# Kernel tuning notes

Hardware: AMD Instinct MI355X
Metric: run time of the kernel (lower is better)

## Reference

```python
import jax, jax.numpy as jnp
import numpy as np

ALPHA = 0.99
EPS = 1e-12
INIT_HI = -60.0
INIT_LO = -90.0
VAR0 = 40.0 ** 2


def setup_inputs() -> dict:
    key = jax.random.key(0)
    x = jax.random.normal(key, (256, 4000, 64), dtype=jnp.float32)
    return {"x": x}


def reference(x) -> jnp.ndarray:
    B, T, F = x.shape
    step = (INIT_LO - INIT_HI) / (F - 1)
    mu0 = INIT_HI + jnp.arange(F, dtype=x.dtype) * step          # [F]
    mu0 = jnp.broadcast_to(mu0[None, :], (B, F))                  # [B, F]
    var0 = jnp.full((B, F), VAR0, dtype=x.dtype)

    def scan_step(carry, xt):
        mu, var = carry
        mu = ALPHA * mu + (1.0 - ALPHA) * xt
        var = ALPHA * var + (1.0 - ALPHA) * (xt - mu) ** 2        # dynamic_var=True
        out = (xt - mu) / (jnp.sqrt(var) + EPS)
        return (mu, var), out

    xt_seq = jnp.swapaxes(x, 0, 1)                                # [T, B, F]
    _, out_seq = jax.lax.scan(scan_step, (mu0, var0), xt_seq)
    return jnp.swapaxes(out_seq, 0, 1)                            # [B, T, F]
```

## Files before the change

kernel.cpp:

```cpp
#include <hip/hip_runtime.h>
#include <math.h>

#define ALPHA   0.99f
#define ONE_M   0.01f
#define T_LEN   4000
#define F_DIM   64
#define TT      160
#define NTILE   25
#define LTC     5
#define NC      32
#define NPC     5
#define NTHREADS 512
#define ROWF    68

typedef float f32x4 __attribute__((ext_vector_type(4)));

#define LGKM_BAR()                                                    \
  do { asm volatile("s_waitcnt lgkmcnt(0)" ::: "memory");             \
       __builtin_amdgcn_sched_barrier(0);                             \
       __builtin_amdgcn_s_barrier();                                  \
       __builtin_amdgcn_sched_barrier(0); } while (0)

#define TILE_BODY(VC, VN, kk)                                               \
  {                                                                         \
    const size_t tb = bbase + (size_t)(kk) * TT * F_DIM;                    \
                    \
    _Pragma("unroll")                                                       \
    for (int r = 0; r < NPC; ++r) {                                         \
      const int t = r * NC + c;                                             \
      *(f32x4*)&s_img[t * ROWF + g * 4] = VC[r];                            \
    }                                                                       \
    LGKM_BAR();                                                             \
    \
    f32x4 vX[LTC];                                                          \
    _Pragma("unroll")                                                       \
    for (int j = 0; j < LTC; ++j)                                           \
      vX[j] = *(const f32x4*)&s_img[(LTC * c + j) * ROWF + g * 4];          \
    if ((kk) + 1 < NTILE) {                                                 \
      _Pragma("unroll")                                                     \
      for (int r = 0; r < NPC; ++r)                                         \
        VN[r] = *(const f32x4*)(x + tb + (size_t)TT * F_DIM                 \
                                + (size_t)tid * 4 + (size_t)r * 2048);      \
    }                                                                       \
    f32x4 m = 0.f, sp = 0.f, su = 0.f;                                      \
    _Pragma("unroll")                                                       \
    for (int j = 0; j < LTC; ++j) {                                         \
      f32x4 xi = vX[j];                                                     \
      m = ALPHA * m + ONE_M * xi;                                           \
      f32x4 u = xi - m;                                                     \
      sp = ALPHA * sp + ONE_M * (u * u);                                    \
      su = su + u;                                                          \
    }                                                                       \
    *(f32x4*)&s_m [c * F_DIM + g * 4] = m;                                  \
    *(f32x4*)&s_sp[c * F_DIM + g * 4] = sp;                                 \
    *(f32x4*)&s_su[c * F_DIM + g * 4] = su;                                 \
    LGKM_BAR();                                                             \
       \
    if (tid < F_DIM) {                                                      \
      float mu = cmu, var = cvar;                                           \
      for (int cc = 0; cc < NC; ++cc) {                                     \
        float mm = s_m [cc * F_DIM + tid];                                  \
        float pp = s_sp[cc * F_DIM + tid];                                  \
        float uu = s_su[cc * F_DIM + tid];                                  \
        s_m [cc * F_DIM + tid] = mu;                    \
        s_sp[cc * F_DIM + tid] = var;                                       \
        float mun = AL * mu + mm;                                           \
        var = AL * var + pp + (C2 * uu) * mu + RR * mu * mu;                \
        mu = mun;                                                           \
      }                                                                     \
      cmu = mu; cvar = var;                                                 \
    }                                                                       \
    LGKM_BAR();                                                             \
     \
    f32x4 mu2  = *(const f32x4*)&s_m [c * F_DIM + g * 4];                   \
    f32x4 var2 = *(const f32x4*)&s_sp[c * F_DIM + g * 4];                   \
    _Pragma("unroll")                                                       \
    for (int j = 0; j < LTC; ++j) {                                         \
      f32x4 xi = vX[j];                                                     \
      mu2 = ALPHA * mu2 + ONE_M * xi;                                       \
      f32x4 d = xi - mu2;                                                   \
      var2 = ALPHA * var2 + ONE_M * (d * d);                                \
      f32x4 o;                                                              \
      o[0] = d[0] * __builtin_amdgcn_rsqf(var2[0]);                         \
      o[1] = d[1] * __builtin_amdgcn_rsqf(var2[1]);                         \
      o[2] = d[2] * __builtin_amdgcn_rsqf(var2[2]);                         \
      o[3] = d[3] * __builtin_amdgcn_rsqf(var2[3]);                         \
      *(f32x4*)&s_img[(LTC * c + j) * ROWF + g * 4] = o;                    \
    }                                                                       \
    LGKM_BAR();                                                             \
            \
    _Pragma("unroll")                                                       \
    for (int r = 0; r < NPC; ++r) {                                         \
      const int t = r * NC + c;                                             \
      f32x4 oc = *(const f32x4*)&s_img[t * ROWF + g * 4];                   \
      *(f32x4*)(out + tb + (size_t)tid * 4 + (size_t)r * 2048) = oc;        \
    }                                                                       \
    LGKM_BAR();           \
  }

__global__ __launch_bounds__(NTHREADS, 2)
void erbnorm_kernel(const float* __restrict__ x, float* __restrict__ out, float aL) {
    const int b   = blockIdx.x;
    const int tid = threadIdx.x;
    const int c   = tid >> 4;
    const int g   = tid & 15;

    const float AL = aL;
    const float C2 = -2.f * ONE_M * aL;
    const float RR = ALPHA * aL * (1.f - aL);

    __shared__ __align__(16) float s_img[TT * ROWF];
    __shared__ float s_m [NC * F_DIM];
    __shared__ float s_sp[NC * F_DIM];
    __shared__ float s_su[NC * F_DIM];

    const size_t bbase = (size_t)b * T_LEN * F_DIM;

    float cmu  = -60.f + (float)tid * (-30.f / 63.f);
    float cvar = 1600.f;

    f32x4 vA[NPC], vB[NPC];
#pragma unroll
    for (int r = 0; r < NPC; ++r)
        vA[r] = *(const f32x4*)(x + bbase + (size_t)tid * 4 + (size_t)r * 2048);

    for (int k2 = 0; k2 < NTILE - 1; k2 += 2) {
        TILE_BODY(vA, vB, k2);
        TILE_BODY(vB, vA, k2 + 1);
    }
    TILE_BODY(vA, vB, NTILE - 1);
}

extern "C" void kernel_launch(void* const* d_in, const int* in_sizes, int n_in,
                              void* d_out, int out_size, void* d_ws, size_t ws_size,
                              hipStream_t stream) {
    const float* x = (const float*)d_in[0];
    float* out = (float*)d_out;
    const float aL = (float)pow(0.99, (double)LTC);
    hipLaunchKernelGGL(erbnorm_kernel, dim3(256), dim3(NTHREADS), 0, stream,
                       x, out, aL);
}
```

Baseline: 110.4 us.

## Give each wave a private LDS slab to replace block barriers with wave fences

The global load/store mapping is rearranged so each wave handles a contiguous 20-timestep slab that matches the 4 chunks it scans. The transpose through LDS can then use a per-wave slab with only a wave-local lgkmcnt wait, which removes two block-wide barriers per tile. The next-tile prefetch is issued at the top of the tile, and launch bounds now ask for 4 blocks per CU. The raised occupancy target may force register spilling, and only the two barriers around the serial cross-chunk scan remain.

```diff
diff --git a/kernel.cpp b/kernel.cpp
--- a/kernel.cpp
+++ b/kernel.cpp
@@ -12,6 +12,7 @@
 #define NPC     5
 #define NTHREADS 512
 #define ROWF    68
+#define SLABF   (20 * ROWF)
 
 typedef float f32x4 __attribute__((ext_vector_type(4)));
 
@@ -21,27 +22,30 @@
        __builtin_amdgcn_s_barrier();                                  \
        __builtin_amdgcn_sched_barrier(0); } while (0)
 
+#define WAVE_FENCE()                                                  \
+  do { asm volatile("s_waitcnt lgkmcnt(0)" ::: "memory");             \
+       __builtin_amdgcn_sched_barrier(0); } while (0)
+
 #define TILE_BODY(VC, VN, kk)                                               \
   {                                                                         \
     const size_t tb = bbase + (size_t)(kk) * TT * F_DIM;                    \
-                    \
+     \
+    if ((kk) + 1 < NTILE) {                                                 \
+      _Pragma("unroll")                                                     \
+      for (int r = 0; r < NPC; ++r)                                         \
+        VN[r] = *(const f32x4*)(x + tb + (size_t)TT * F_DIM + woff          \
+                                + (size_t)r * 256 + (size_t)lw * 4);        \
+    }                                                                       \
+                        \
     _Pragma("unroll")                                                       \
-    for (int r = 0; r < NPC; ++r) {                                         \
-      const int t = r * NC + c;                                             \
-      *(f32x4*)&s_img[t * ROWF + g * 4] = VC[r];                            \
-    }                                                                       \
-    LGKM_BAR();                                                             \
-    \
+    for (int r = 0; r < NPC; ++r)                                           \
+      *(f32x4*)&slab[(4 * r + cl) * ROWF + g * 4] = VC[r];                  \
+    WAVE_FENCE();                \
+     \
     f32x4 vX[LTC];                                                          \
     _Pragma("unroll")                                                       \
     for (int j = 0; j < LTC; ++j)                                           \
-      vX[j] = *(const f32x4*)&s_img[(LTC * c + j) * ROWF + g * 4];          \
-    if ((kk) + 1 < NTILE) {                                                 \
-      _Pragma("unroll")                                                     \
-      for (int r = 0; r < NPC; ++r)                                         \
-        VN[r] = *(const f32x4*)(x + tb + (size_t)TT * F_DIM                 \
-                                + (size_t)tid * 4 + (size_t)r * 2048);      \
-    }                                                                       \
+      vX[j] = *(const f32x4*)&slab[(LTC * cl + j) * ROWF + g * 4];          \
     f32x4 m = 0.f, sp = 0.f, su = 0.f;                                      \
     _Pragma("unroll")                                                       \
     for (int j = 0; j < LTC; ++j) {                                         \
@@ -54,7 +58,7 @@
     *(f32x4*)&s_m [c * F_DIM + g * 4] = m;                                  \
     *(f32x4*)&s_sp[c * F_DIM + g * 4] = sp;                                 \
     *(f32x4*)&s_su[c * F_DIM + g * 4] = su;                                 \
-    LGKM_BAR();                                                             \
+    LGKM_BAR();                            \
        \
     if (tid < F_DIM) {                                                      \
       float mu = cmu, var = cvar;                                           \
@@ -70,7 +74,7 @@
       }                                                                     \
       cmu = mu; cvar = var;                                                 \
     }                                                                       \
-    LGKM_BAR();                                                             \
+    LGKM_BAR();                          \
      \
     f32x4 mu2  = *(const f32x4*)&s_m [c * F_DIM + g * 4];                   \
     f32x4 var2 = *(const f32x4*)&s_sp[c * F_DIM + g * 4];                   \
@@ -85,34 +89,38 @@
       o[1] = d[1] * __builtin_amdgcn_rsqf(var2[1]);                         \
       o[2] = d[2] * __builtin_amdgcn_rsqf(var2[2]);                         \
       o[3] = d[3] * __builtin_amdgcn_rsqf(var2[3]);                         \
-      *(f32x4*)&s_img[(LTC * c + j) * ROWF + g * 4] = o;                    \
+      *(f32x4*)&slab[(LTC * cl + j) * ROWF + g * 4] = o;                    \
     }                                                                       \
-    LGKM_BAR();                                                             \
-            \
+    WAVE_FENCE();                \
+     \
     _Pragma("unroll")                                                       \
     for (int r = 0; r < NPC; ++r) {                                         \
-      const int t = r * NC + c;                                             \
-      f32x4 oc = *(const f32x4*)&s_img[t * ROWF + g * 4];                   \
-      *(f32x4*)(out + tb + (size_t)tid * 4 + (size_t)r * 2048) = oc;        \
+      f32x4 oc = *(const f32x4*)&slab[(4 * r + cl) * ROWF + g * 4];         \
+      *(f32x4*)(out + tb + woff + (size_t)r * 256 + (size_t)lw * 4) = oc;   \
     }                                                                       \
-    LGKM_BAR();           \
+    WAVE_FENCE();       \
   }
 
-__global__ __launch_bounds__(NTHREADS, 2)
+__global__ __launch_bounds__(NTHREADS, 4)
 void erbnorm_kernel(const float* __restrict__ x, float* __restrict__ out, float aL) {
     const int b   = blockIdx.x;
     const int tid = threadIdx.x;
+    const int w   = tid >> 6;
+    const int lw  = tid & 63;
     const int c   = tid >> 4;
+    const int cl  = (tid >> 4) & 3;
     const int g   = tid & 15;
+    const size_t woff = (size_t)w * 1280;
 
     const float AL = aL;
     const float C2 = -2.f * ONE_M * aL;
     const float RR = ALPHA * aL * (1.f - aL);
 
-    __shared__ __align__(16) float s_img[TT * ROWF];
+    __shared__ __align__(16) float lds_img[8 * SLABF];
     __shared__ float s_m [NC * F_DIM];
     __shared__ float s_sp[NC * F_DIM];
     __shared__ float s_su[NC * F_DIM];
+    float* slab = &lds_img[w * SLABF];
 
     const size_t bbase = (size_t)b * T_LEN * F_DIM;
 
@@ -122,7 +130,7 @@
     f32x4 vA[NPC], vB[NPC];
 #pragma unroll
     for (int r = 0; r < NPC; ++r)
-        vA[r] = *(const f32x4*)(x + bbase + (size_t)tid * 4 + (size_t)r * 2048);
+        vA[r] = *(const f32x4*)(x + bbase + woff + (size_t)r * 256 + (size_t)lw * 4);
 
     for (int k2 = 0; k2 < NTILE - 1; k2 += 2) {
         TILE_BODY(vA, vB, k2);
```

New measurement: 144.2 us. 1.31x slower.
